# Kernel tuning notes

Measured on AMD Instinct MI355X. Metric: run time of the kernel, lower is better.

The kernel has to match this reference:

```python
import jax, jax.numpy as jnp
import numpy as np

NH, NP, C = 12, 4, 768           # heads, points, d_model
HD = C // NH                      # head dim (deform_ratio=1.0)
SHAPES = np.array([[128, 128], [64, 64], [32, 32]], dtype=np.int64)
LSI = np.array([0, 128 * 128, 128 * 128 + 64 * 64], dtype=np.int64)
L = SHAPES.shape[0]
EPS = 1e-6


def setup_inputs() -> dict:
    key = jax.random.key(0)
    ks = jax.random.split(key, 10)
    N, Lq = 4, 64 * 64
    Lin = int((SHAPES[:, 0] * SHAPES[:, 1]).sum())
    s = 0.02
    return {
        "query": jax.random.normal(ks[0], (N, Lq, C), jnp.float32),
        "reference_points": jax.random.uniform(ks[1], (N, Lq, L, 2), dtype=jnp.float32),
        "feat": jax.random.normal(ks[2], (N, Lin, C), jnp.float32),
        "qnorm_w": jnp.ones((C,), jnp.float32),
        "qnorm_b": jnp.zeros((C,), jnp.float32),
        "fnorm_w": jnp.ones((C,), jnp.float32),
        "fnorm_b": jnp.zeros((C,), jnp.float32),
        "gamma": jnp.full((C,), 0.01, jnp.float32),
        "so_w": s * jax.random.normal(ks[3], (C, NH * L * NP * 2), jnp.float32),
        "so_b": s * jax.random.normal(ks[4], (NH * L * NP * 2,), jnp.float32),
        "aw_w": s * jax.random.normal(ks[5], (C, NH * L * NP), jnp.float32),
        "aw_b": s * jax.random.normal(ks[6], (NH * L * NP,), jnp.float32),
        "vp_w": s * jax.random.normal(ks[7], (C, C), jnp.float32),
        "vp_b": jnp.zeros((C,), jnp.float32),
        "op_w": s * jax.random.normal(ks[8], (C, C), jnp.float32),
        "op_b": jnp.zeros((C,), jnp.float32),
        "spatial_shapes": SHAPES,
        "level_start_index": LSI,
    }


def _ln(x, w, b):
    mu = x.mean(-1, keepdims=True)
    var = ((x - mu) ** 2).mean(-1, keepdims=True)
    return (x - mu) * jax.lax.rsqrt(var + EPS) * w + b


def reference(query, reference_points, feat, qnorm_w, qnorm_b, fnorm_w, fnorm_b,
              gamma, so_w, so_b, aw_w, aw_b, vp_w, vp_b, op_w, op_b,
              spatial_shapes, level_start_index):
    N, Lq, C_ = query.shape
    ss = np.asarray(spatial_shapes)
    lsi = np.asarray(level_start_index)
    q = _ln(query, qnorm_w, qnorm_b)
    f = _ln(feat, fnorm_w, fnorm_b)
    # value projection -> [N, nh, Lin, hd]
    value = (f @ vp_w + vp_b).reshape(N, -1, NH, HD).transpose(0, 2, 1, 3)
    off = (q @ so_w + so_b).reshape(N, Lq, NH, L, NP, 2)
    aw = jax.nn.softmax((q @ aw_w + aw_b).reshape(N, Lq, NH, L * NP), axis=-1)
    aw = aw.reshape(N, Lq, NH, L, NP)
    # offset normalizer is (W, H) per level
    offset_norm = jnp.asarray(ss[:, ::-1].copy(), jnp.float32)
    loc = reference_points[:, :, None, :, None, :] + off / offset_norm[None, None, None, :, None, :]
    out = jnp.zeros((N, Lq, NH, HD), query.dtype)
    for l in range(L):
        H_, W_ = int(ss[l, 0]), int(ss[l, 1])
        st = int(lsi[l])
        v = value[:, :, st:st + H_ * W_, :]                     # [N,nh,HW,hd]
        ll = loc[:, :, :, l].transpose(0, 2, 1, 3, 4).reshape(N, NH, Lq * NP, 2)
        # grid_sample, align_corners=False: map [0,1] -> pixel coords
        px = ll[..., 0] * W_ - 0.5
        py = ll[..., 1] * H_ - 0.5
        x0 = jnp.floor(px)
        y0 = jnp.floor(py)
        tx = px - x0
        ty = py - y0
        x0i = x0.astype(jnp.int32)
        y0i = y0.astype(jnp.int32)
        acc = jnp.zeros((N, NH, Lq * NP, HD), query.dtype)
        for dx, dy, w in ((0, 0, (1 - tx) * (1 - ty)), (1, 0, tx * (1 - ty)),
                          (0, 1, (1 - tx) * ty), (1, 1, tx * ty)):
            xi = x0i + dx
            yi = y0i + dy
            ok = (xi >= 0) & (xi < W_) & (yi >= 0) & (yi < H_)  # zero padding
            idx = jnp.clip(yi, 0, H_ - 1) * W_ + jnp.clip(xi, 0, W_ - 1)
            g = jnp.take_along_axis(v, idx[..., None], axis=2)   # [N,nh,Lq*P,hd]
            acc = acc + g * (w * ok)[..., None]
        samp = acc.reshape(N, NH, Lq, NP, HD)
        out = out + jnp.einsum('nhqpd,nqhp->nqhd', samp, aw[:, :, :, l])
    attn = out.reshape(N, Lq, C_) @ op_w + op_b
    return query + gamma * attn
```

## Files before the change

kernel.cpp:

```cpp
#include <hip/hip_runtime.h>
#include <hip/hip_bf16.h>
#include <stdint.h>

#define NHD   12
#define NPT   4
#define CDIM  768
#define HDIM  64
#define NLVL  3
#define LQ    4096
#define NB    4
#define LIN   21504
#define MQ    (NB*LQ)
#define MF    (NB*LIN)
#define CAT_N 512
#define AW_OFF 288
#define WSCL  16.f

typedef float  f32x4  __attribute__((ext_vector_type(4)));
typedef float  f32x2  __attribute__((ext_vector_type(2)));
typedef float  f32x16 __attribute__((ext_vector_type(16)));
typedef int    i32x8  __attribute__((ext_vector_type(8)));

__device__ __forceinline__ i32x8 mk8(uint4 lo, uint4 hi) {
  i32x8 v;
  v[0] = (int)lo.x; v[1] = (int)lo.y; v[2] = (int)lo.z; v[3] = (int)lo.w;
  v[4] = (int)hi.x; v[5] = (int)hi.y; v[6] = (int)hi.z; v[7] = (int)hi.w;
  return v;
}

__global__ __launch_bounds__(256) void prep_weights(
    const float* __restrict__ vp_w, const float* __restrict__ op_w,
    const float* __restrict__ so_w, const float* __restrict__ aw_w,
    const float* __restrict__ so_b, const float* __restrict__ aw_b,
    char* __restrict__ vp_w8, char* __restrict__ op_w8,
    char* __restrict__ cat_w8, float* __restrict__ cat_bp)
{
  const int b = blockIdx.x;
  if (b == 1536) {
    const int i = threadIdx.x;
#pragma unroll
    for (int it = 0; it < 2; ++it) {
      const int idx = i + it * 256;
      float v = 0.f;
      if (idx < 288) v = so_b[idx];
      else if (idx < 432) v = aw_b[idx - AW_OFF];
      cat_bp[idx] = v;
    }
    return;
  }
  const float* W; char* Wt; int Nsrc, rowoff; float scale;
  int lb;
  if (b < 576)       { W = vp_w; Wt = vp_w8;  Nsrc = 768; rowoff = 0;   scale = 1.f;  lb = b; }
  else if (b < 1152) { W = op_w; Wt = op_w8;  Nsrc = 768; rowoff = 0;   scale = 1.f;  lb = b - 576; }
  else if (b < 1368) { W = so_w; Wt = cat_w8; Nsrc = 288; rowoff = 0;   scale = WSCL; lb = b - 1152; }
  else               { W = aw_w; Wt = cat_w8; Nsrc = 144; rowoff = 288; scale = WSCL; lb = b - 1368; }

  __shared__ float t[32][33];
  const int k0 = (lb % 24) * 32;
  const int n0 = (lb / 24) * 32;
  const int tx = threadIdx.x & 31, ty = threadIdx.x >> 5;
#pragma unroll
  for (int i = ty; i < 32; i += 8) {
    const int n = n0 + tx;
    t[i][tx] = (n < Nsrc) ? W[(size_t)(k0 + i) * Nsrc + n] * scale : 0.f;
  }
  __syncthreads();
#pragma unroll
  for (int i = ty; i < 32; i += 8) {
    const int n = rowoff + n0 + i;
    uint32_t pk = __builtin_amdgcn_cvt_pk_fp8_f32(t[tx][i], 0.f, 0, false);
    Wt[(size_t)n * CDIM + k0 + tx] = (char)(pk & 0xff);
  }
}

__global__ __launch_bounds__(256) void ln_wave2(
    const float* __restrict__ xq, const float* __restrict__ wq,
    const float* __restrict__ bq, char* __restrict__ yq,
    const float* __restrict__ xf, const float* __restrict__ wf,
    const float* __restrict__ bf, char* __restrict__ yf)
{
  const float* x; const float* w; const float* b; char* y; int row;
  if (blockIdx.x < MQ / 4) {
    x = xq; w = wq; b = bq; y = yq;
    row = blockIdx.x * 4 + (threadIdx.x >> 6);
  } else {
    x = xf; w = wf; b = bf; y = yf;
    row = (blockIdx.x - MQ / 4) * 4 + (threadIdx.x >> 6);
  }
  const int lane = threadIdx.x & 63;
  const float4* xr = (const float4*)(x + (size_t)row * CDIM);
  float4 v[3];
  v[0] = xr[lane]; v[1] = xr[lane + 64]; v[2] = xr[lane + 128];
  float s1 = 0.f, s2 = 0.f;
#pragma unroll
  for (int i = 0; i < 3; ++i) {
    s1 += v[i].x + v[i].y + v[i].z + v[i].w;
    s2 += v[i].x*v[i].x + v[i].y*v[i].y + v[i].z*v[i].z + v[i].w*v[i].w;
  }
#pragma unroll
  for (int o = 32; o > 0; o >>= 1) { s1 += __shfl_xor(s1, o); s2 += __shfl_xor(s2, o); }
  const float mu = s1 * (1.f / CDIM);
  const float rs = rsqrtf(s2 * (1.f / CDIM) - mu * mu + 1e-6f);
#pragma unroll
  for (int i = 0; i < 3; ++i) {
    const float4 w4 = ((const float4*)w)[lane + i * 64];
    const float4 b4 = ((const float4*)b)[lane + i * 64];
    const float o0 = (v[i].x - mu) * rs * w4.x + b4.x;
    const float o1 = (v[i].y - mu) * rs * w4.y + b4.y;
    const float o2 = (v[i].z - mu) * rs * w4.z + b4.z;
    const float o3 = (v[i].w - mu) * rs * w4.w + b4.w;
    uint32_t pk = 0;
    pk = __builtin_amdgcn_cvt_pk_fp8_f32(o0, o1, pk, false);
    pk = __builtin_amdgcn_cvt_pk_fp8_f32(o2, o3, pk, true);
    ((uint32_t*)(y + (size_t)row * CDIM))[lane + i * 64] = pk;
  }
}

template<int MODE>
__global__ __launch_bounds__(256, 3) void gemm_mx(
    const char* __restrict__ A, const char* __restrict__ Wt,
    const float* __restrict__ bias, void* __restrict__ Cout,
    int M, int N, int K, int nTN, float oscale,
    const float* __restrict__ resid, const float* __restrict__ gammav)
{
  __shared__ __align__(16) char lds[49152];

  int bid = blockIdx.x;
  const int nwg = gridDim.x;
  if ((nwg & 7) == 0) {
    const int chunk = nwg >> 3;
    bid = (bid & 7) * chunk + (bid >> 3);
  }
  const int mt = bid / nTN, ntl = bid - mt * nTN;
  const int m0 = mt * 128, n0 = ntl * 128;
  const int tid  = threadIdx.x;
  const int lane = tid & 63, wid = tid >> 6;
  const int wm = wid >> 1, wn = wid & 1;
  const int lr31 = lane & 31, lkb = lane >> 5;

  f32x16 acc[2][2] = {};

  auto stage = [&](int kt, int buf, int ab) {
    const char* srcM = ab ? Wt : A;
    const int base0 = ab ? n0 : m0;
    const int k0 = kt * 64;
    char* dst0 = lds + buf * 16384 + ab * 8192;
#pragma unroll
    for (int it = 0; it < 2; ++it) {
      const int i = it * 256 + tid;
      const int r = i >> 2, p = i & 3;
      const int c = p ^ (r & 3);
      const char* src = srcM + (size_t)(base0 + r) * K + k0 + c * 16;
      char* dst = dst0 + (it * 256 + wid * 64) * 16;
      __builtin_amdgcn_global_load_lds(
          (const __attribute__((address_space(1))) uint32_t*)src,
          (__attribute__((address_space(3))) uint32_t*)dst, 16, 0, 0);
    }
  };
  auto rdop = [&](int buf, int ab, int row) -> i32x8 {
    const char* base = lds + buf * 16384 + ab * 8192 + row * 64;
    const int s = row & 3;
    const uint4 lo = *(const uint4*)(base + ((2 * lkb)     ^ s) * 16);
    const uint4 hi = *(const uint4*)(base + ((2 * lkb + 1) ^ s) * 16);
    return mk8(lo, hi);
  };

  const int nk = K >> 6;
  stage(0, 0, 0); stage(0, 0, 1);
  stage(1, 1, 0); stage(1, 1, 1);
  asm volatile("s_waitcnt vmcnt(4)" ::: "memory");
  __builtin_amdgcn_s_barrier();
  asm volatile("" ::: "memory");

  for (int t = 0; t < nk; ++t) {
    const int cur = t % 3;
    const i32x8 a0 = rdop(cur, 0, wm * 64 + lr31);
    const i32x8 a1 = rdop(cur, 0, wm * 64 + 32 + lr31);
    const i32x8 b0 = rdop(cur, 1, wn * 64 + lr31);
    const i32x8 b1 = rdop(cur, 1, wn * 64 + 32 + lr31);
    if (t + 2 < nk) { const int tb = (t + 2) % 3; stage(t + 2, tb, 0); stage(t + 2, tb, 1); }
    __builtin_amdgcn_s_setprio(1);
    acc[0][0] = __builtin_amdgcn_mfma_scale_f32_32x32x64_f8f6f4(
        a0, b0, acc[0][0], 0, 0, 0, 0x7F7F7F7F, 0, 0x7F7F7F7F);
    acc[0][1] = __builtin_amdgcn_mfma_scale_f32_32x32x64_f8f6f4(
        a0, b1, acc[0][1], 0, 0, 0, 0x7F7F7F7F, 0, 0x7F7F7F7F);
    acc[1][0] = __builtin_amdgcn_mfma_scale_f32_32x32x64_f8f6f4(
        a1, b0, acc[1][0], 0, 0, 0, 0x7F7F7F7F, 0, 0x7F7F7F7F);
    acc[1][1] = __builtin_amdgcn_mfma_scale_f32_32x32x64_f8f6f4(
        a1, b1, acc[1][1], 0, 0, 0, 0x7F7F7F7F, 0, 0x7F7F7F7F);
    __builtin_amdgcn_s_setprio(0);
    if (t + 2 < nk)      asm volatile("s_waitcnt vmcnt(4)" ::: "memory");
    else if (t + 1 < nk) asm volatile("s_waitcnt vmcnt(0)" ::: "memory");
    __builtin_amdgcn_s_barrier();
    asm volatile("" ::: "memory");
  }

  if constexpr (MODE == 0) {
    const int head  = (n0 + wn * 64) >> 6;
    const int n_img = (unsigned)m0 / LIN;
    char* plane = (char*)Cout + ((size_t)(n_img * NHD + head) * LIN
                                 + (m0 - n_img * LIN)) * 64;
    float bcol[2];
#pragma unroll
    for (int nt2 = 0; nt2 < 2; ++nt2)
      bcol[nt2] = bias[n0 + wn * 64 + nt2 * 32 + lr31];
    float* my = (float*)(lds + wid * 8704);
#pragma unroll
    for (int mt2 = 0; mt2 < 2; ++mt2) {
#pragma unroll
      for (int nt2 = 0; nt2 < 2; ++nt2)
#pragma unroll
        for (int reg = 0; reg < 16; ++reg) {
          const int row = (reg & 3) + 8 * (reg >> 2) + 4 * lkb;
          my[row * 68 + nt2 * 32 + lr31] = acc[mt2][nt2][reg] + bcol[nt2];
        }
#pragma unroll
      for (int it = 0; it < 2; ++it) {
        const int idx = it * 64 + lane;
        const int row = idx >> 2, seg = idx & 3;
        const float* s = my + row * 68 + seg * 16;
        uint32_t w[4];
#pragma unroll
        for (int q = 0; q < 4; ++q) {
          uint32_t pk = 0;
          pk = __builtin_amdgcn_cvt_pk_fp8_f32(s[q*4+0], s[q*4+1], pk, false);
          pk = __builtin_amdgcn_cvt_pk_fp8_f32(s[q*4+2], s[q*4+3], pk, true);
          w[q] = pk;
        }
        char* orow = plane + (size_t)(wm * 64 + mt2 * 32 + row) * 64 + seg * 16;
        *(uint4*)orow = *(uint4*)w;
      }
    }
  } else {
#pragma unroll
    for (int nt2 = 0; nt2 < 2; ++nt2) {
      const int col = n0 + wn * 64 + nt2 * 32 + lr31;
      const float bcol = bias[col];
      float gcol = 0.f;
      if constexpr (MODE == 2) gcol = gammav[col];
#pragma unroll
      for (int mt2 = 0; mt2 < 2; ++mt2)
#pragma unroll
        for (int reg = 0; reg < 16; ++reg) {
          const int row = m0 + wm * 64 + mt2 * 32
                        + (reg & 3) + 8 * (reg >> 2) + 4 * lkb;
          const size_t o = (size_t)row * N + col;
          if constexpr (MODE == 1)
            ((float*)Cout)[o] = acc[mt2][nt2][reg] * oscale + bcol;
          else
            ((float*)Cout)[o] = resid[o] + gcol * (acc[mt2][nt2][reg] + bcol);
        }
    }
  }
}

__global__ void softmax_pack(const float* __restrict__ raw,
                             const float* __restrict__ refp,
                             float4* __restrict__ params) {
  const int t = blockIdx.x * 256 + threadIdx.x;
  const int h = t % NHD, nq = t / NHD;
  const float* p = raw + (size_t)nq * CAT_N + AW_OFF + h * 12;
  float v[12], m = -1e30f;
#pragma unroll
  for (int j = 0; j < 12; ++j) { v[j] = p[j]; m = fmaxf(m, v[j]); }
  float s = 0.f;
#pragma unroll
  for (int j = 0; j < 12; ++j) { v[j] = __expf(v[j] - m); s += v[j]; }
  const float inv = 1.f / s;
  const float* op = raw + (size_t)nq * CAT_N + h * 24;
  const float* rp = refp + (size_t)nq * (NLVL * 2);
  float4* out = params + (size_t)t * 12;
  const float Wf[3] = {128.f, 64.f, 32.f};
#pragma unroll
  for (int l = 0; l < NLVL; ++l) {
    const float rxw = rp[2 * l] * Wf[l] - 0.5f;
    const float ryw = rp[2 * l + 1] * Wf[l] - 0.5f;
#pragma unroll
    for (int pt = 0; pt < NPT; ++pt) {
      float4 o4;
      o4.x = rxw + op[(l * 4 + pt) * 2 + 0];
      o4.y = ryw + op[(l * 4 + pt) * 2 + 1];
      o4.z = v[l * 4 + pt] * inv;
      o4.w = 0.f;
      out[l * 4 + pt] = o4;
    }
  }
}

__global__ __launch_bounds__(256) void deform_grp16(
    const char* __restrict__ vbytes, const float4* __restrict__ params,
    char* __restrict__ samp)
{
  const int j = blockIdx.x;
  const int x = j & 7, k = j >> 3;
  const int g = x + ((k >> 6) << 3);
  const int i = k & 63;
  const int n = g / NHD, h = g - n * NHD;
  const int wid = threadIdx.x >> 6, lane = threadIdx.x & 63;
  const int qi = lane >> 2, ci = lane & 3;
  const int q  = i * 64 + wid * 16 + qi;
  const int nq = n * LQ + q;
  const float4* __restrict__ pp = params + ((size_t)nq * NHD + h) * 12;
  const uint32_t base0 = (uint32_t)g * (uint32_t)(LIN * 64)
                       + ((uint32_t)ci << 4);

  float acc[16];
#pragma unroll
  for (int c = 0; c < 16; ++c) acc[c] = 0.f;

  const int      Wl[3]  = {128, 64, 32};
  const uint32_t STb[3] = {0u, 16384u * 64u, 20480u * 64u};

#pragma unroll
  for (int l = 0; l < NLVL; ++l) {
    const int W_ = Wl[l];
    const uint32_t base = base0 + STb[l];
#pragma unroll
    for (int p = 0; p < NPT; ++p) {
      const float4 pt = pp[l * 4 + p];
      const float fx = floorf(pt.x), fy = floorf(pt.y);
      const float tx = pt.x - fx,   ty = pt.y - fy;
      const int x0 = (int)fx, y0 = (int)fy;
      const int x1 = x0 + 1,  y1 = y0 + 1;
      const float wx0 = ((uint32_t)x0 < (uint32_t)W_) ? (1.f - tx) : 0.f;
      const float wx1 = ((uint32_t)x1 < (uint32_t)W_) ? tx : 0.f;
      const float wy0 = ((uint32_t)y0 < (uint32_t)W_) ? pt.z * (1.f - ty) : 0.f;
      const float wy1 = ((uint32_t)y1 < (uint32_t)W_) ? pt.z * ty : 0.f;
      const int xc0 = min(max(x0, 0), W_ - 1);
      const int xc1 = min(max(x1, 0), W_ - 1);
      const int yr0 = min(max(y0, 0), W_ - 1) * W_;
      const int yr1 = min(max(y1, 0), W_ - 1) * W_;
      const float cw[4] = {wy0 * wx0, wy0 * wx1, wy1 * wx0, wy1 * wx1};
      const uint4 G0 = *(const uint4*)(vbytes + base + (uint32_t)(yr0 + xc0) * 64u);
      const uint4 G1 = *(const uint4*)(vbytes + base + (uint32_t)(yr0 + xc1) * 64u);
      const uint4 G2 = *(const uint4*)(vbytes + base + (uint32_t)(yr1 + xc0) * 64u);
      const uint4 G3 = *(const uint4*)(vbytes + base + (uint32_t)(yr1 + xc1) * 64u);
      const uint4 GG[4] = {G0, G1, G2, G3};
#pragma unroll
      for (int cnr = 0; cnr < 4; ++cnr) {
        const uint32_t wds[4] = {GG[cnr].x, GG[cnr].y, GG[cnr].z, GG[cnr].w};
        const float wgt = cw[cnr];
#pragma unroll
        for (int wd = 0; wd < 4; ++wd) {
          f32x2 lo = __builtin_amdgcn_cvt_pk_f32_fp8(wds[wd], false);
          f32x2 hi = __builtin_amdgcn_cvt_pk_f32_fp8(wds[wd], true);
          acc[wd * 4 + 0] += lo[0] * wgt;
          acc[wd * 4 + 1] += lo[1] * wgt;
          acc[wd * 4 + 2] += hi[0] * wgt;
          acc[wd * 4 + 3] += hi[1] * wgt;
        }
      }
    }
  }

  uint32_t out[4];
#pragma unroll
  for (int wd = 0; wd < 4; ++wd) {
    uint32_t pk = 0;
    pk = __builtin_amdgcn_cvt_pk_fp8_f32(acc[wd*4+0], acc[wd*4+1], pk, false);
    pk = __builtin_amdgcn_cvt_pk_fp8_f32(acc[wd*4+2], acc[wd*4+3], pk, true);
    out[wd] = pk;
  }
  *(uint4*)(samp + (size_t)nq * CDIM + h * HDIM + ci * 16) = *(uint4*)out;
}

extern "C" void kernel_launch(void* const* d_in, const int* in_sizes, int n_in,
                              void* d_out, int out_size, void* d_ws, size_t ws_size,
                              hipStream_t stream) {
  const float* query = (const float*)d_in[0];
  const float* refp  = (const float*)d_in[1];
  const float* feat  = (const float*)d_in[2];
  const float* qn_w  = (const float*)d_in[3];
  const float* qn_b  = (const float*)d_in[4];
  const float* fn_w  = (const float*)d_in[5];
  const float* fn_b  = (const float*)d_in[6];
  const float* gamma = (const float*)d_in[7];
  const float* so_w  = (const float*)d_in[8];
  const float* so_b  = (const float*)d_in[9];
  const float* aw_w  = (const float*)d_in[10];
  const float* aw_b  = (const float*)d_in[11];
  const float* vp_w  = (const float*)d_in[12];
  const float* vp_b  = (const float*)d_in[13];
  const float* op_w  = (const float*)d_in[14];
  const float* op_b  = (const float*)d_in[15];

  char* ws = (char*)d_ws;
  size_t off = 0;
  auto alloc = [&](size_t bytes) {
    char* p = ws + off;
    off = (off + bytes + 255) & ~(size_t)255;
    return p;
  };
  char*   q_f8   = (char*)alloc((size_t)MQ * CDIM);
  char*   val_f8 = (char*)alloc((size_t)MF * CDIM);
  char*   vp_w8  = (char*)alloc((size_t)CDIM * CDIM);
  char*   op_w8  = (char*)alloc((size_t)CDIM * CDIM);
  char*   cat_w8 = (char*)alloc((size_t)CAT_N * CDIM);
  float*  cat_bp = (float*)alloc(CAT_N * 4);

  const size_t r = off;
  char* f_f8 = ws + r;
  const size_t f_end = r + (size_t)MF * CDIM;
  size_t o2 = r;
  float*  raw     = (float*)(ws + o2);  o2 += (size_t)MQ * CAT_N * 4;
  float4* params  = (float4*)(ws + o2); o2 += (size_t)MQ * NHD * 12 * 16;
  char*   samp8   = (char*)(ws + o2);   o2 += (size_t)MQ * CDIM;
  const size_t need = (f_end > o2) ? f_end : o2;
  if (ws_size < need) return;

  prep_weights<<<1537, 256, 0, stream>>>(vp_w, op_w, so_w, aw_w, so_b, aw_b,
                                         vp_w8, op_w8, cat_w8, cat_bp);

  ln_wave2<<<(MQ + MF) / 4, 256, 0, stream>>>(query, qn_w, qn_b, q_f8,
                                              feat, fn_w, fn_b, f_f8);

  gemm_mx<0><<<(MF / 128) * (CDIM / 128), 256, 0, stream>>>(
      f_f8, vp_w8, vp_b, val_f8, MF, CDIM, CDIM, CDIM / 128,
      1.f, nullptr, nullptr);

  gemm_mx<1><<<(MQ / 128) * (CAT_N / 128), 256, 0, stream>>>(
      q_f8, cat_w8, cat_bp, raw, MQ, CAT_N, CDIM, CAT_N / 128,
      1.f / WSCL, nullptr, nullptr);

  softmax_pack<<<(MQ * NHD) / 256, 256, 0, stream>>>(raw, refp, params);

  deform_grp16<<<48 * 64, 256, 0, stream>>>(val_f8, params, samp8);

  gemm_mx<2><<<(MQ / 128) * (CDIM / 128), 256, 0, stream>>>(
      samp8, op_w8, op_b, (float*)d_out, MQ, CDIM, CDIM, CDIM / 128,
      1.f, query, gamma);
}
```

Measured before the change: 271.5 us.

## Fuse weight prep with layernorm and softmax/param packing into deform kernel

Merges the weight-conversion kernel and the layernorm kernel into one launch by splitting block ranges, and moves softmax and sampling-parameter packing into the deformable sampling kernel, which stages the parameters in LDS. This removes two kernel launches and the global round-trip of the params buffer (about 12 MB written then read). In exchange, each deform block now runs a serial prologue on one wave plus a barrier before sampling, and reads the raw projection rows directly.

```diff
diff --git a/kernel.cpp b/kernel.cpp
--- a/kernel.cpp
+++ b/kernel.cpp
@@ -15,6 +15,7 @@
 #define CAT_N 512
 #define AW_OFF 288
 #define WSCL  16.f
+#define PREP_NB 1537
 
 typedef float  f32x4  __attribute__((ext_vector_type(4)));
 typedef float  f32x2  __attribute__((ext_vector_type(2)));
@@ -28,14 +29,58 @@
   return v;
 }
 
-__global__ __launch_bounds__(256) void prep_weights(
+__global__ __launch_bounds__(256) void prep_and_ln(
     const float* __restrict__ vp_w, const float* __restrict__ op_w,
     const float* __restrict__ so_w, const float* __restrict__ aw_w,
     const float* __restrict__ so_b, const float* __restrict__ aw_b,
     char* __restrict__ vp_w8, char* __restrict__ op_w8,
-    char* __restrict__ cat_w8, float* __restrict__ cat_bp)
+    char* __restrict__ cat_w8, float* __restrict__ cat_bp,
+    const float* __restrict__ xq, const float* __restrict__ wq,
+    const float* __restrict__ bq, char* __restrict__ yq,
+    const float* __restrict__ xf, const float* __restrict__ wf,
+    const float* __restrict__ bf, char* __restrict__ yf)
 {
-  const int b = blockIdx.x;
+  const int blk = blockIdx.x;
+  if (blk >= PREP_NB) {
+    const int lb = blk - PREP_NB;
+    const float* x; const float* w; const float* b; char* y; int row;
+    if (lb < MQ / 4) {
+      x = xq; w = wq; b = bq; y = yq;
+      row = lb * 4 + (threadIdx.x >> 6);
+    } else {
+      x = xf; w = wf; b = bf; y = yf;
+      row = (lb - MQ / 4) * 4 + (threadIdx.x >> 6);
+    }
+    const int lane = threadIdx.x & 63;
+    const float4* xr = (const float4*)(x + (size_t)row * CDIM);
+    float4 v[3];
+    v[0] = xr[lane]; v[1] = xr[lane + 64]; v[2] = xr[lane + 128];
+    float s1 = 0.f, s2 = 0.f;
+#pragma unroll
+    for (int i = 0; i < 3; ++i) {
+      s1 += v[i].x + v[i].y + v[i].z + v[i].w;
+      s2 += v[i].x*v[i].x + v[i].y*v[i].y + v[i].z*v[i].z + v[i].w*v[i].w;
+    }
+#pragma unroll
+    for (int o = 32; o > 0; o >>= 1) { s1 += __shfl_xor(s1, o); s2 += __shfl_xor(s2, o); }
+    const float mu = s1 * (1.f / CDIM);
+    const float rs = rsqrtf(s2 * (1.f / CDIM) - mu * mu + 1e-6f);
+#pragma unroll
+    for (int i = 0; i < 3; ++i) {
+      const float4 w4 = ((const float4*)w)[lane + i * 64];
+      const float4 b4 = ((const float4*)b)[lane + i * 64];
+      const float o0 = (v[i].x - mu) * rs * w4.x + b4.x;
+      const float o1 = (v[i].y - mu) * rs * w4.y + b4.y;
+      const float o2 = (v[i].z - mu) * rs * w4.z + b4.z;
+      const float o3 = (v[i].w - mu) * rs * w4.w + b4.w;
+      uint32_t pk = 0;
+      pk = __builtin_amdgcn_cvt_pk_fp8_f32(o0, o1, pk, false);
+      pk = __builtin_amdgcn_cvt_pk_fp8_f32(o2, o3, pk, true);
+      ((uint32_t*)(y + (size_t)row * CDIM))[lane + i * 64] = pk;
+    }
+    return;
+  }
+  const int b = blk;
   if (b == 1536) {
     const int i = threadIdx.x;
 #pragma unroll
@@ -70,49 +115,6 @@
     const int n = rowoff + n0 + i;
     uint32_t pk = __builtin_amdgcn_cvt_pk_fp8_f32(t[tx][i], 0.f, 0, false);
     Wt[(size_t)n * CDIM + k0 + tx] = (char)(pk & 0xff);
-  }
-}
-
-__global__ __launch_bounds__(256) void ln_wave2(
-    const float* __restrict__ xq, const float* __restrict__ wq,
-    const float* __restrict__ bq, char* __restrict__ yq,
-    const float* __restrict__ xf, const float* __restrict__ wf,
-    const float* __restrict__ bf, char* __restrict__ yf)
-{
-  const float* x; const float* w; const float* b; char* y; int row;
-  if (blockIdx.x < MQ / 4) {
-    x = xq; w = wq; b = bq; y = yq;
-    row = blockIdx.x * 4 + (threadIdx.x >> 6);
-  } else {
-    x = xf; w = wf; b = bf; y = yf;
-    row = (blockIdx.x - MQ / 4) * 4 + (threadIdx.x >> 6);
-  }
-  const int lane = threadIdx.x & 63;
-  const float4* xr = (const float4*)(x + (size_t)row * CDIM);
-  float4 v[3];
-  v[0] = xr[lane]; v[1] = xr[lane + 64]; v[2] = xr[lane + 128];
-  float s1 = 0.f, s2 = 0.f;
-#pragma unroll
-  for (int i = 0; i < 3; ++i) {
-    s1 += v[i].x + v[i].y + v[i].z + v[i].w;
-    s2 += v[i].x*v[i].x + v[i].y*v[i].y + v[i].z*v[i].z + v[i].w*v[i].w;
-  }
-#pragma unroll
-  for (int o = 32; o > 0; o >>= 1) { s1 += __shfl_xor(s1, o); s2 += __shfl_xor(s2, o); }
-  const float mu = s1 * (1.f / CDIM);
-  const float rs = rsqrtf(s2 * (1.f / CDIM) - mu * mu + 1e-6f);
-#pragma unroll
-  for (int i = 0; i < 3; ++i) {
-    const float4 w4 = ((const float4*)w)[lane + i * 64];
-    const float4 b4 = ((const float4*)b)[lane + i * 64];
-    const float o0 = (v[i].x - mu) * rs * w4.x + b4.x;
-    const float o1 = (v[i].y - mu) * rs * w4.y + b4.y;
-    const float o2 = (v[i].z - mu) * rs * w4.z + b4.z;
-    const float o3 = (v[i].w - mu) * rs * w4.w + b4.w;
-    uint32_t pk = 0;
-    pk = __builtin_amdgcn_cvt_pk_fp8_f32(o0, o1, pk, false);
-    pk = __builtin_amdgcn_cvt_pk_fp8_f32(o2, o3, pk, true);
-    ((uint32_t*)(y + (size_t)row * CDIM))[lane + i * 64] = pk;
   }
 }
 
@@ -254,53 +256,57 @@
   }
 }
 
-__global__ void softmax_pack(const float* __restrict__ raw,
-                             const float* __restrict__ refp,
-                             float4* __restrict__ params) {
-  const int t = blockIdx.x * 256 + threadIdx.x;
-  const int h = t % NHD, nq = t / NHD;
-  const float* p = raw + (size_t)nq * CAT_N + AW_OFF + h * 12;
-  float v[12], m = -1e30f;
-#pragma unroll
-  for (int j = 0; j < 12; ++j) { v[j] = p[j]; m = fmaxf(m, v[j]); }
-  float s = 0.f;
-#pragma unroll
-  for (int j = 0; j < 12; ++j) { v[j] = __expf(v[j] - m); s += v[j]; }
-  const float inv = 1.f / s;
-  const float* op = raw + (size_t)nq * CAT_N + h * 24;
-  const float* rp = refp + (size_t)nq * (NLVL * 2);
-  float4* out = params + (size_t)t * 12;
-  const float Wf[3] = {128.f, 64.f, 32.f};
-#pragma unroll
-  for (int l = 0; l < NLVL; ++l) {
-    const float rxw = rp[2 * l] * Wf[l] - 0.5f;
-    const float ryw = rp[2 * l + 1] * Wf[l] - 0.5f;
-#pragma unroll
-    for (int pt = 0; pt < NPT; ++pt) {
-      float4 o4;
-      o4.x = rxw + op[(l * 4 + pt) * 2 + 0];
-      o4.y = ryw + op[(l * 4 + pt) * 2 + 1];
-      o4.z = v[l * 4 + pt] * inv;
-      o4.w = 0.f;
-      out[l * 4 + pt] = o4;
-    }
-  }
-}
-
-__global__ __launch_bounds__(256) void deform_grp16(
-    const char* __restrict__ vbytes, const float4* __restrict__ params,
-    char* __restrict__ samp)
+__global__ __launch_bounds__(256) void deform_fused(
+    const char* __restrict__ vbytes, const float* __restrict__ raw,
+    const float* __restrict__ refp, char* __restrict__ samp)
 {
   const int j = blockIdx.x;
   const int x = j & 7, k = j >> 3;
   const int g = x + ((k >> 6) << 3);
   const int i = k & 63;
   const int n = g / NHD, h = g - n * NHD;
+  const int q0 = i * 64;
+
+  __shared__ float4 pp_lds[64][12];
+
+  if (threadIdx.x < 64) {
+    const int nq = n * LQ + q0 + threadIdx.x;
+    const float* praw = raw + (size_t)nq * CAT_N;
+    float v[12], m = -1e30f;
+#pragma unroll
+    for (int jj = 0; jj < 12; ++jj) {
+      v[jj] = praw[AW_OFF + h * 12 + jj];
+      m = fmaxf(m, v[jj]);
+    }
+    float s = 0.f;
+#pragma unroll
+    for (int jj = 0; jj < 12; ++jj) { v[jj] = __expf(v[jj] - m); s += v[jj]; }
+    const float inv = 1.f / s;
+    const float* op = praw + h * 24;
+    const float* rp = refp + (size_t)nq * (NLVL * 2);
+    const float Wf[3] = {128.f, 64.f, 32.f};
+#pragma unroll
+    for (int l = 0; l < NLVL; ++l) {
+      const float rxw = rp[2 * l] * Wf[l] - 0.5f;
+      const float ryw = rp[2 * l + 1] * Wf[l] - 0.5f;
+#pragma unroll
+      for (int pt = 0; pt < NPT; ++pt) {
+        float4 o4;
+        o4.x = rxw + op[(l * 4 + pt) * 2 + 0];
+        o4.y = ryw + op[(l * 4 + pt) * 2 + 1];
+        o4.z = v[l * 4 + pt] * inv;
+        o4.w = 0.f;
+        pp_lds[threadIdx.x][l * 4 + pt] = o4;
+      }
+    }
+  }
+  __syncthreads();
+
   const int wid = threadIdx.x >> 6, lane = threadIdx.x & 63;
   const int qi = lane >> 2, ci = lane & 3;
-  const int q  = i * 64 + wid * 16 + qi;
-  const int nq = n * LQ + q;
-  const float4* __restrict__ pp = params + ((size_t)nq * NHD + h) * 12;
+  const int ql = wid * 16 + qi;
+  const int nq = n * LQ + q0 + ql;
+  const float4* __restrict__ pp = pp_lds[ql];
   const uint32_t base0 = (uint32_t)g * (uint32_t)(LIN * 64)
                        + ((uint32_t)ci << 4);
 
@@ -403,16 +409,13 @@
   const size_t f_end = r + (size_t)MF * CDIM;
   size_t o2 = r;
   float*  raw     = (float*)(ws + o2);  o2 += (size_t)MQ * CAT_N * 4;
-  float4* params  = (float4*)(ws + o2); o2 += (size_t)MQ * NHD * 12 * 16;
   char*   samp8   = (char*)(ws + o2);   o2 += (size_t)MQ * CDIM;
   const size_t need = (f_end > o2) ? f_end : o2;
   if (ws_size < need) return;
 
-  prep_weights<<<1537, 256, 0, stream>>>(vp_w, op_w, so_w, aw_w, so_b, aw_b,
-                                         vp_w8, op_w8, cat_w8, cat_bp);
-
-  ln_wave2<<<(MQ + MF) / 4, 256, 0, stream>>>(query, qn_w, qn_b, q_f8,
-                                              feat, fn_w, fn_b, f_f8);
+  prep_and_ln<<<PREP_NB + (MQ + MF) / 4, 256, 0, stream>>>(
+      vp_w, op_w, so_w, aw_w, so_b, aw_b, vp_w8, op_w8, cat_w8, cat_bp,
+      query, qn_w, qn_b, q_f8, feat, fn_w, fn_b, f_f8);
 
   gemm_mx<0><<<(MF / 128) * (CDIM / 128), 256, 0, stream>>>(
       f_f8, vp_w8, vp_b, val_f8, MF, CDIM, CDIM, CDIM / 128,
@@ -422,9 +425,7 @@
       q_f8, cat_w8, cat_bp, raw, MQ, CAT_N, CDIM, CAT_N / 128,
       1.f / WSCL, nullptr, nullptr);
 
-  softmax_pack<<<(MQ * NHD) / 256, 256, 0, stream>>>(raw, refp, params);
-
-  deform_grp16<<<48 * 64, 256, 0, stream>>>(val_f8, params, samp8);
+  deform_fused<<<48 * 64, 256, 0, stream>>>(val_f8, raw, refp, samp8);
 
   gemm_mx<2><<<(MQ / 128) * (CDIM / 128), 256, 0, stream>>>(
       samp8, op_w8, op_b, (float*)d_out, MQ, CDIM, CDIM, CDIM / 128,
```

New measurement: 240.0 us. 11.6% less time.
